# Kernel optimization log

Measured on AMD Instinct MI355X. Metric: run time of the kernel, lower is better.

## Reference

```python
import jax, jax.numpy as jnp
import numpy as np

B, N, T, F = 16, 512, 24, 64


def setup_inputs() -> dict:
    key = jax.random.key(0)
    k1, k2, k3, k4 = jax.random.split(key, 4)
    ori_flow = jax.random.normal(k1, (B, N, T, F), dtype=jnp.float32)
    uncer = jax.random.normal(k2, (B, N, T, F), dtype=jnp.float32)
    spatial_embedding = jax.random.normal(k3, (N, F), dtype=jnp.float32)
    # nn.Linear(channels, channels, bias=False): y = x @ W.T, W: (out, in)
    W1 = jax.random.normal(k4, (F, F), dtype=jnp.float32) * (1.0 / np.sqrt(F))
    return {"ori_flow": ori_flow, "uncer": uncer,
            "spatial_embedding": spatial_embedding, "W1": W1}


def reference(ori_flow, uncer, spatial_embedding, W1):
    b, n, t, f = ori_flow.shape
    # (B, N, T, f) -> (B*T, N, f)
    x = ori_flow.transpose(0, 2, 1, 3).reshape(-1, n, f)
    u = uncer.transpose(0, 2, 1, 3).reshape(-1, n, f)
    # spatial embedding is identical across batch and time after expand/permute
    emb = jnp.broadcast_to(spatial_embedding, (b * t, n, f))
    h = jnp.concatenate([x, emb], axis=-1)            # (B*T, N, 2f)
    rel = jax.nn.relu(jnp.einsum('bnf,bmf->bnm', h, h))  # (B*T, N, N)
    rel = jax.nn.softmax(rel, axis=-1)                # dropout p=0 -> identity
    # sharing_paras=True: both branches use linear1 (no bias)
    of = jax.nn.relu(jnp.einsum('bnm,bmf->bnf', rel, x) @ W1.T)
    uf = jax.nn.relu(jnp.einsum('bnm,bmf->bnf', rel, u) @ W1.T)
    of = of.reshape(b, t, n, f).transpose(0, 2, 1, 3)  # (B, N, T, f)
    uf = uf.reshape(b, t, n, f).transpose(0, 2, 1, 3)
    return of, uf
```

## Files before the change

### kernel.cpp

```cpp
#include <hip/hip_runtime.h>
#include <hip/hip_bf16.h>

#define BB 16
#define NN 512
#define TT 24
#define FF 64
#define OUT_OFF ((size_t)BB*NN*TT*FF)

#define AIS 136
#define XTS 72
#define XTSZ 4672

typedef __attribute__((ext_vector_type(8))) short v8s;
typedef __attribute__((ext_vector_type(16))) float v16f;

union U16x8 { uint4 v; unsigned short s[8]; };

__device__ inline v16f mfma32(v8s a, v8s b, v16f c) {
    return __builtin_amdgcn_mfma_f32_32x32x16_bf16(a, b, c, 0, 0, 0);
}

__device__ inline unsigned int fbits(float x) {
    union { float f; unsigned int u; } c; c.f = x; return c.u;
}
__device__ inline float ibits(unsigned int u) {
    union { float f; unsigned int u; } c; c.u = u; return c.f;
}
__device__ inline unsigned short f2bf_r(float x) {
    return (unsigned short)((fbits(x) + 0x8000u) >> 16);
}
__device__ inline float bf2f(unsigned short u) {
    return ibits(((unsigned int)u) << 16);
}
__device__ inline void split8(const float* f, U16x8& H, U16x8& L) {
    #pragma unroll
    for (int k = 0; k < 8; ++k) {
        unsigned int u  = fbits(f[k]);
        unsigned int hr = (u + 0x8000u) & 0xffff0000u;
        H.s[k] = (unsigned short)(hr >> 16);
        float lo = f[k] - ibits(hr);
        L.s[k] = (unsigned short)((fbits(lo) + 0x8000u) >> 16);
    }
}
__device__ inline void cvt8h(const float* f, U16x8& H) {
    #pragma unroll
    for (int k = 0; k < 8; ++k) H.s[k] = f2bf_r(f[k]);
}

__device__ inline unsigned int pkbf(float a, float b) {
    unsigned int r;
    asm("v_cvt_pk_bf16_f32 %0, %1, %2" : "=v"(r) : "v"(a), "v"(b));
    return r;
}

__device__ inline v8s pfrag(const float* cr, int c) {
    unsigned int a0 = pkbf(cr[8*c+0], cr[8*c+1]);
    unsigned int a1 = pkbf(cr[8*c+2], cr[8*c+3]);
    unsigned int b0 = pkbf(cr[8*c+4], cr[8*c+5]);
    unsigned int b1 = pkbf(cr[8*c+6], cr[8*c+7]);
    asm("v_permlane32_swap_b32 %0, %1" : "+v"(a0), "+v"(b0));
    asm("v_permlane32_swap_b32 %0, %1" : "+v"(a1), "+v"(b1));
    union { v8s v; unsigned int u[4]; } P;
    P.u[0] = a0; P.u[1] = a1; P.u[2] = b0; P.u[3] = b1;
    return P.v;
}

__global__ __launch_bounds__(256, 2)
void spag_kernel(const float* __restrict__ ori, const float* __restrict__ unc,
                 const float* __restrict__ emb, const float* __restrict__ W1,
                 float* __restrict__ out)
{
    __shared__ __align__(16) unsigned short SH[2*64*AIS + 2*XTSZ];
    unsigned short* AjH = SH;
    unsigned short* AjL = SH + 64*AIS;
    unsigned short* XT  = SH + 2*64*AIS;
    unsigned short* UT  = XT + XTSZ;

    const int tid  = threadIdx.x;
    const int bt   = blockIdx.x >> 2;
    const int it   = blockIdx.x & 3;
    const int b    = bt / TT, t = bt % TT;
    const int i0   = it * 128;

    const int lane = tid & 63;
    const int w    = tid >> 6;
    const int m    = lane & 31;
    const int hi   = lane >> 5;

    v8s bH[8], bL[8];
    #pragma unroll
    for (int p = 0; p < 2; ++p) {
        {
            const int sr = tid >> 2, fc = (tid & 3) * 16;
            const float* xb = ori + ((size_t)((b*NN + i0 + p*64 + sr)*TT + t))*FF + fc;
            const float* eb = emb + (size_t)(i0 + p*64 + sr)*FF + fc;
            float tf[8]; U16x8 H, L;
            #pragma unroll
            for (int h = 0; h < 2; ++h) {
                *(float4*)&tf[0] = ((const float4*)xb)[2*h];
                *(float4*)&tf[4] = ((const float4*)xb)[2*h+1];
                split8(tf, H, L);
                *(uint4*)&AjH[sr*AIS + fc + h*8] = H.v;
                *(uint4*)&AjL[sr*AIS + fc + h*8] = L.v;
                *(float4*)&tf[0] = ((const float4*)eb)[2*h];
                *(float4*)&tf[4] = ((const float4*)eb)[2*h+1];
                split8(tf, H, L);
                *(uint4*)&AjH[sr*AIS + 64 + fc + h*8] = H.v;
                *(uint4*)&AjL[sr*AIS + 64 + fc + h*8] = L.v;
            }
        }
        __syncthreads();
        if ((w >> 1) == p) {
            const int lr = (w & 1)*32 + m;
            #pragma unroll
            for (int kk = 0; kk < 8; ++kk) {
                bH[kk] = *(const v8s*)&AjH[lr*AIS + kk*16 + hi*8];
                bL[kk] = *(const v8s*)&AjL[lr*AIS + kk*16 + hi*8];
            }
        }
        __syncthreads();
    }

    v16f accX0 = (v16f)(0.0f), accX1 = (v16f)(0.0f);
    v16f accU0 = (v16f)(0.0f), accU1 = (v16f)(0.0f);
    float rs    = 0.0f;
    float m_run = 0.0f;

    for (int jt = 0; jt < 8; ++jt) {
        const int j0 = jt * 64;
        __syncthreads();

        {
            const int pj = tid >> 3;
            const int f0 = (tid & 7) * 8;
            const int j  = 2 * pj;
            const size_t r0 = ((size_t)((b*NN + j0 + j)*TT + t))*FF + f0;
            const size_t r1 = r0 + (size_t)TT*FF;
            float t0[8], t1[8]; U16x8 H0, L0, H1, L1;

            *(float4*)&t0[0] = *(const float4*)(ori + r0);
            *(float4*)&t0[4] = *(const float4*)(ori + r0 + 4);
            *(float4*)&t1[0] = *(const float4*)(ori + r1);
            *(float4*)&t1[4] = *(const float4*)(ori + r1 + 4);
            split8(t0, H0, L0); split8(t1, H1, L1);
            *(uint4*)&AjH[ j   *AIS + f0] = H0.v;
            *(uint4*)&AjH[(j+1)*AIS + f0] = H1.v;
            *(uint4*)&AjL[ j   *AIS + f0] = L0.v;
            *(uint4*)&AjL[(j+1)*AIS + f0] = L1.v;
            #pragma unroll
            for (int k = 0; k < 8; ++k) {
                int f = f0 + k;
                int off = f*XTS + (f>>4)*16 + j;
                *(unsigned int*)&XT[off] =
                    (unsigned int)H0.s[k] | ((unsigned int)H1.s[k] << 16);
            }
            const float* e0 = emb + (size_t)(j0 + j)*FF + f0;
            *(float4*)&t0[0] = *(const float4*)(e0);
            *(float4*)&t0[4] = *(const float4*)(e0 + 4);
            *(float4*)&t1[0] = *(const float4*)(e0 + FF);
            *(float4*)&t1[4] = *(const float4*)(e0 + FF + 4);
            split8(t0, H0, L0); split8(t1, H1, L1);
            *(uint4*)&AjH[ j   *AIS + 64 + f0] = H0.v;
            *(uint4*)&AjH[(j+1)*AIS + 64 + f0] = H1.v;
            *(uint4*)&AjL[ j   *AIS + 64 + f0] = L0.v;
            *(uint4*)&AjL[(j+1)*AIS + 64 + f0] = L1.v;
            *(float4*)&t0[0] = *(const float4*)(unc + r0);
            *(float4*)&t0[4] = *(const float4*)(unc + r0 + 4);
            *(float4*)&t1[0] = *(const float4*)(unc + r1);
            *(float4*)&t1[4] = *(const float4*)(unc + r1 + 4);
            #pragma unroll
            for (int k = 0; k < 8; ++k) {
                int f = f0 + k;
                int off = f*XTS + (f>>4)*16 + j;
                *(unsigned int*)&UT[off] =
                    (unsigned int)f2bf_r(t0[k]) | ((unsigned int)f2bf_r(t1[k]) << 16);
            }
        }
        __syncthreads();

        v16f C0 = (v16f)(0.0f), C1 = (v16f)(0.0f);
        #pragma unroll
        for (int kk = 0; kk < 8; ++kk) {
            const int fo = kk*16 + hi*8;
            v8s aH0 = *(const v8s*)&AjH[ m     *AIS + fo];
            v8s aL0 = *(const v8s*)&AjL[ m     *AIS + fo];
            v8s aH1 = *(const v8s*)&AjH[(32+m)*AIS + fo];
            v8s aL1 = *(const v8s*)&AjL[(32+m)*AIS + fo];
            C0 = mfma32(aH0, bH[kk], C0);
            C1 = mfma32(aH1, bH[kk], C1);
            C0 = mfma32(aH0, bL[kk], C0);
            C1 = mfma32(aH1, bL[kk], C1);
            C0 = mfma32(aL0, bH[kk], C0);
            C1 = mfma32(aL1, bH[kk], C1);
        }

        float mt = 0.0f;
        #pragma unroll
        for (int r = 0; r < 16; ++r) {
            float s0 = fmaxf(C0[r], 0.0f); C0[r] = s0;
            float s1 = fmaxf(C1[r], 0.0f); C1[r] = s1;
            mt = fmaxf(mt, fmaxf(s0, s1));
        }
        mt = fmaxf(mt, __shfl_xor(mt, 32));
        if (!__all(mt <= m_run + 8.0f)) {
            float m_new = fmaxf(m_run, mt);
            float al = __expf(m_run - m_new);
            rs *= al; m_run = m_new;
            #pragma unroll
            for (int r = 0; r < 16; ++r) {
                float a = __shfl(al, (r & 3) + 8*(r >> 2) + 4*hi);
                accX0[r] *= a; accX1[r] *= a;
                accU0[r] *= a; accU1[r] *= a;
            }
        }

        v8s P[4];
        {
            float cr[16];
            #pragma unroll
            for (int r = 0; r < 16; ++r) {
                float e = __expf(C0[r] - m_run);
                cr[r] = ibits((fbits(e) + 0x8000u) & 0xffff0000u);
                rs += cr[r];
            }
            P[0] = pfrag(cr, 0);
            P[1] = pfrag(cr, 1);
            #pragma unroll
            for (int r = 0; r < 16; ++r) {
                float e = __expf(C1[r] - m_run);
                cr[r] = ibits((fbits(e) + 0x8000u) & 0xffff0000u);
                rs += cr[r];
            }
            P[2] = pfrag(cr, 0);
            P[3] = pfrag(cr, 1);
        }

        #pragma unroll
        for (int kk = 0; kk < 4; ++kk) {
            const int fo = kk*16 + hi*8;
            v8s bx0 = *(const v8s*)&XT[ m     *XTS + (( m    )>>4)*16 + fo];
            v8s bu0 = *(const v8s*)&UT[ m     *XTS + (( m    )>>4)*16 + fo];
            v8s bx1 = *(const v8s*)&XT[(32+m)*XTS + (((32+m))>>4)*16 + fo];
            v8s bu1 = *(const v8s*)&UT[(32+m)*XTS + (((32+m))>>4)*16 + fo];
            accX0 = mfma32(P[kk], bx0, accX0);
            accX1 = mfma32(P[kk], bx1, accX1);
            accU0 = mfma32(P[kk], bu0, accU0);
            accU1 = mfma32(P[kk], bu1, accU1);
        }
    }

    __syncthreads();
    rs += __shfl_xor(rs, 32);
    float inv = 1.0f / rs;

    unsigned short* Ox = SH;
    unsigned short* Ou = SH + 128*XTS;
    unsigned short* Wt = SH + 256*XTS;

    #pragma unroll
    for (int r = 0; r < 16; ++r) {
        int il = (r & 3) + 8*(r >> 2) + 4*hi;
        float iv = __shfl(inv, il);
        int row = w*32 + il;
        Ox[row*XTS + m]      = f2bf_r(accX0[r] * iv);
        Ox[row*XTS + 32 + m] = f2bf_r(accX1[r] * iv);
        Ou[row*XTS + m]      = f2bf_r(accU0[r] * iv);
        Ou[row*XTS + 32 + m] = f2bf_r(accU1[r] * iv);
    }
    {
        const int sr = tid >> 2, fc = (tid & 3) * 16;
        const float* wb = W1 + sr*FF + fc;
        float tf[8]; U16x8 H;
        #pragma unroll
        for (int h = 0; h < 2; ++h) {
            *(float4*)&tf[0] = ((const float4*)wb)[2*h];
            *(float4*)&tf[4] = ((const float4*)wb)[2*h+1];
            cvt8h(tf, H);
            *(uint4*)&Wt[sr*XTS + fc + h*8] = H.v;
        }
    }
    __syncthreads();

    v8s ao[4], aq[4];
    #pragma unroll
    for (int kk = 0; kk < 4; ++kk) {
        const int fo = kk*16 + hi*8;
        ao[kk] = *(const v8s*)&Ox[(w*32 + m)*XTS + fo];
        aq[kk] = *(const v8s*)&Ou[(w*32 + m)*XTS + fo];
    }
    #pragma unroll
    for (int ot = 0; ot < 2; ++ot) {
        v16f ax = (v16f)(0.0f), au = (v16f)(0.0f);
        #pragma unroll
        for (int kk = 0; kk < 4; ++kk) {
            const int fo = kk*16 + hi*8;
            v8s bw = *(const v8s*)&Wt[(ot*32 + m)*XTS + fo];
            ax = mfma32(ao[kk], bw, ax);
            au = mfma32(aq[kk], bw, au);
        }
        #pragma unroll
        for (int r = 0; r < 16; ++r) {
            int il = (r & 3) + 8*(r >> 2) + 4*hi;
            int i = i0 + w*32 + il;
            int o = ot*32 + m;
            size_t idx = ((size_t)((b*NN + i)*TT + t))*FF + o;
            out[idx]           = fmaxf(ax[r], 0.0f);
            out[OUT_OFF + idx] = fmaxf(au[r], 0.0f);
        }
    }
}

extern "C" void kernel_launch(void* const* d_in, const int* in_sizes, int n_in,
                              void* d_out, int out_size, void* d_ws, size_t ws_size,
                              hipStream_t stream) {
    const float* ori = (const float*)d_in[0];
    const float* unc = (const float*)d_in[1];
    const float* emb = (const float*)d_in[2];
    const float* W1  = (const float*)d_in[3];
    float* out = (float*)d_out;

    spag_kernel<<<dim3(BB*TT*4), dim3(256), 0, stream>>>(ori, unc, emb, W1, out);
}
```

Before: 268.2 us.

## Halve j-tile to 32 rows to cut LDS and raise occupancy

Shrinks the key tile from 64 to 32 rows per iteration, halving the shared-memory buffers. The launch bound rises from 2 to 5 blocks per CU and per-thread accumulator state drops. The epilogue is restructured so the W1 projection fits the smaller LDS by processing row halves in two passes. In exchange the main loop runs twice as many iterations with twice as many barriers, and each tile load is smaller.

```diff
diff --git a/kernel.cpp b/kernel.cpp
--- a/kernel.cpp
+++ b/kernel.cpp
@@ -8,13 +8,17 @@
 #define OUT_OFF ((size_t)BB*NN*TT*FF)
 
 #define AIS 136
-#define XTS 72
-#define XTSZ 4672
+#define XTS 56
+#define AJSZ (32*AIS)
+#define XTSZ (64*XTS+16)
+#define OS   72
+#define EOS  (64*OS+16)
 
 typedef __attribute__((ext_vector_type(8))) short v8s;
 typedef __attribute__((ext_vector_type(16))) float v16f;
 
 union U16x8 { uint4 v; unsigned short s[8]; };
+union U16x4 { uint2 v; unsigned short s[4]; };
 
 __device__ inline v16f mfma32(v8s a, v8s b, v16f c) {
     return __builtin_amdgcn_mfma_f32_32x32x16_bf16(a, b, c, 0, 0, 0);
@@ -29,22 +33,15 @@
 __device__ inline unsigned short f2bf_r(float x) {
     return (unsigned short)((fbits(x) + 0x8000u) >> 16);
 }
-__device__ inline float bf2f(unsigned short u) {
-    return ibits(((unsigned int)u) << 16);
-}
-__device__ inline void split8(const float* f, U16x8& H, U16x8& L) {
+__device__ inline void split4(const float* f, U16x4& H, U16x4& L) {
     #pragma unroll
-    for (int k = 0; k < 8; ++k) {
+    for (int k = 0; k < 4; ++k) {
         unsigned int u  = fbits(f[k]);
         unsigned int hr = (u + 0x8000u) & 0xffff0000u;
         H.s[k] = (unsigned short)(hr >> 16);
         float lo = f[k] - ibits(hr);
         L.s[k] = (unsigned short)((fbits(lo) + 0x8000u) >> 16);
     }
-}
-__device__ inline void cvt8h(const float* f, U16x8& H) {
-    #pragma unroll
-    for (int k = 0; k < 8; ++k) H.s[k] = f2bf_r(f[k]);
 }
 
 __device__ inline unsigned int pkbf(float a, float b) {
@@ -65,15 +62,15 @@
     return P.v;
 }
 
-__global__ __launch_bounds__(256, 2)
+__global__ __launch_bounds__(256, 5)
 void spag_kernel(const float* __restrict__ ori, const float* __restrict__ unc,
                  const float* __restrict__ emb, const float* __restrict__ W1,
                  float* __restrict__ out)
 {
-    __shared__ __align__(16) unsigned short SH[2*64*AIS + 2*XTSZ];
+    __shared__ __align__(16) unsigned short SH[2*AJSZ + 2*XTSZ];
     unsigned short* AjH = SH;
-    unsigned short* AjL = SH + 64*AIS;
-    unsigned short* XT  = SH + 2*64*AIS;
+    unsigned short* AjL = SH + AJSZ;
+    unsigned short* XT  = SH + 2*AJSZ;
     unsigned short* UT  = XT + XTSZ;
 
     const int tid  = threadIdx.x;
@@ -87,35 +84,38 @@
     const int m    = lane & 31;
     const int hi   = lane >> 5;
 
+    const int pr = tid >> 4;
+    const int f0 = (tid & 15) * 4;
+    const int jl = 2 * pr;
+
     v8s bH[8], bL[8];
     #pragma unroll
-    for (int p = 0; p < 2; ++p) {
+    for (int p = 0; p < 4; ++p) {
         {
-            const int sr = tid >> 2, fc = (tid & 3) * 16;
-            const float* xb = ori + ((size_t)((b*NN + i0 + p*64 + sr)*TT + t))*FF + fc;
-            const float* eb = emb + (size_t)(i0 + p*64 + sr)*FF + fc;
-            float tf[8]; U16x8 H, L;
-            #pragma unroll
-            for (int h = 0; h < 2; ++h) {
-                *(float4*)&tf[0] = ((const float4*)xb)[2*h];
-                *(float4*)&tf[4] = ((const float4*)xb)[2*h+1];
-                split8(tf, H, L);
-                *(uint4*)&AjH[sr*AIS + fc + h*8] = H.v;
-                *(uint4*)&AjL[sr*AIS + fc + h*8] = L.v;
-                *(float4*)&tf[0] = ((const float4*)eb)[2*h];
-                *(float4*)&tf[4] = ((const float4*)eb)[2*h+1];
-                split8(tf, H, L);
-                *(uint4*)&AjH[sr*AIS + 64 + fc + h*8] = H.v;
-                *(uint4*)&AjL[sr*AIS + 64 + fc + h*8] = L.v;
-            }
-        }
-        __syncthreads();
-        if ((w >> 1) == p) {
-            const int lr = (w & 1)*32 + m;
+            const int gi = i0 + p*32 + jl;
+            const float* xb = ori + ((size_t)((b*NN + gi)*TT + t))*FF + f0;
+            const float* eb = emb + (size_t)gi*FF + f0;
+            float a0[4], a1[4], e0[4], e1[4];
+            *(float4*)a0 = *(const float4*)xb;
+            *(float4*)a1 = *(const float4*)(xb + (size_t)TT*FF);
+            *(float4*)e0 = *(const float4*)eb;
+            *(float4*)e1 = *(const float4*)(eb + FF);
+            U16x4 H, L;
+            split4(a0, H, L);
+            *(uint2*)&AjH[ jl   *AIS + f0] = H.v;  *(uint2*)&AjL[ jl   *AIS + f0] = L.v;
+            split4(a1, H, L);
+            *(uint2*)&AjH[(jl+1)*AIS + f0] = H.v;  *(uint2*)&AjL[(jl+1)*AIS + f0] = L.v;
+            split4(e0, H, L);
+            *(uint2*)&AjH[ jl   *AIS + 64 + f0] = H.v;  *(uint2*)&AjL[ jl   *AIS + 64 + f0] = L.v;
+            split4(e1, H, L);
+            *(uint2*)&AjH[(jl+1)*AIS + 64 + f0] = H.v;  *(uint2*)&AjL[(jl+1)*AIS + 64 + f0] = L.v;
+        }
+        __syncthreads();
+        if (w == p) {
             #pragma unroll
             for (int kk = 0; kk < 8; ++kk) {
-                bH[kk] = *(const v8s*)&AjH[lr*AIS + kk*16 + hi*8];
-                bL[kk] = *(const v8s*)&AjL[lr*AIS + kk*16 + hi*8];
+                bH[kk] = *(const v8s*)&AjH[m*AIS + kk*16 + hi*8];
+                bL[kk] = *(const v8s*)&AjL[m*AIS + kk*16 + hi*8];
             }
         }
         __syncthreads();
@@ -126,80 +126,63 @@
     float rs    = 0.0f;
     float m_run = 0.0f;
 
-    for (int jt = 0; jt < 8; ++jt) {
-        const int j0 = jt * 64;
+    for (int jt = 0; jt < 16; ++jt) {
+        const int j0 = jt * 32;
         __syncthreads();
 
         {
-            const int pj = tid >> 3;
-            const int f0 = (tid & 7) * 8;
-            const int j  = 2 * pj;
-            const size_t r0 = ((size_t)((b*NN + j0 + j)*TT + t))*FF + f0;
+            const int gj = j0 + jl;
+            const size_t r0 = ((size_t)((b*NN + gj)*TT + t))*FF + f0;
             const size_t r1 = r0 + (size_t)TT*FF;
-            float t0[8], t1[8]; U16x8 H0, L0, H1, L1;
-
-            *(float4*)&t0[0] = *(const float4*)(ori + r0);
-            *(float4*)&t0[4] = *(const float4*)(ori + r0 + 4);
-            *(float4*)&t1[0] = *(const float4*)(ori + r1);
-            *(float4*)&t1[4] = *(const float4*)(ori + r1 + 4);
-            split8(t0, H0, L0); split8(t1, H1, L1);
-            *(uint4*)&AjH[ j   *AIS + f0] = H0.v;
-            *(uint4*)&AjH[(j+1)*AIS + f0] = H1.v;
-            *(uint4*)&AjL[ j   *AIS + f0] = L0.v;
-            *(uint4*)&AjL[(j+1)*AIS + f0] = L1.v;
-            #pragma unroll
-            for (int k = 0; k < 8; ++k) {
+            const float* ep = emb + (size_t)gj*FF + f0;
+            float a0[4], a1[4], e0[4], e1[4], u0[4], u1[4];
+            *(float4*)a0 = *(const float4*)(ori + r0);
+            *(float4*)a1 = *(const float4*)(ori + r1);
+            *(float4*)e0 = *(const float4*)(ep);
+            *(float4*)e1 = *(const float4*)(ep + FF);
+            *(float4*)u0 = *(const float4*)(unc + r0);
+            *(float4*)u1 = *(const float4*)(unc + r1);
+
+            U16x4 H0, L0, H1, L1;
+            split4(a0, H0, L0); split4(a1, H1, L1);
+            *(uint2*)&AjH[ jl   *AIS + f0] = H0.v;  *(uint2*)&AjL[ jl   *AIS + f0] = L0.v;
+            *(uint2*)&AjH[(jl+1)*AIS + f0] = H1.v;  *(uint2*)&AjL[(jl+1)*AIS + f0] = L1.v;
+            #pragma unroll
+            for (int k = 0; k < 4; ++k) {
                 int f = f0 + k;
-                int off = f*XTS + (f>>4)*16 + j;
+                int off = f*XTS + ((f>>4)&1)*16 + jl;
                 *(unsigned int*)&XT[off] =
                     (unsigned int)H0.s[k] | ((unsigned int)H1.s[k] << 16);
             }
-            const float* e0 = emb + (size_t)(j0 + j)*FF + f0;
-            *(float4*)&t0[0] = *(const float4*)(e0);
-            *(float4*)&t0[4] = *(const float4*)(e0 + 4);
-            *(float4*)&t1[0] = *(const float4*)(e0 + FF);
-            *(float4*)&t1[4] = *(const float4*)(e0 + FF + 4);
-            split8(t0, H0, L0); split8(t1, H1, L1);
-            *(uint4*)&AjH[ j   *AIS + 64 + f0] = H0.v;
-            *(uint4*)&AjH[(j+1)*AIS + 64 + f0] = H1.v;
-            *(uint4*)&AjL[ j   *AIS + 64 + f0] = L0.v;
-            *(uint4*)&AjL[(j+1)*AIS + 64 + f0] = L1.v;
-            *(float4*)&t0[0] = *(const float4*)(unc + r0);
-            *(float4*)&t0[4] = *(const float4*)(unc + r0 + 4);
-            *(float4*)&t1[0] = *(const float4*)(unc + r1);
-            *(float4*)&t1[4] = *(const float4*)(unc + r1 + 4);
-            #pragma unroll
-            for (int k = 0; k < 8; ++k) {
+            split4(e0, H0, L0); split4(e1, H1, L1);
+            *(uint2*)&AjH[ jl   *AIS + 64 + f0] = H0.v;  *(uint2*)&AjL[ jl   *AIS + 64 + f0] = L0.v;
+            *(uint2*)&AjH[(jl+1)*AIS + 64 + f0] = H1.v;  *(uint2*)&AjL[(jl+1)*AIS + 64 + f0] = L1.v;
+            #pragma unroll
+            for (int k = 0; k < 4; ++k) {
                 int f = f0 + k;
-                int off = f*XTS + (f>>4)*16 + j;
+                int off = f*XTS + ((f>>4)&1)*16 + jl;
                 *(unsigned int*)&UT[off] =
-                    (unsigned int)f2bf_r(t0[k]) | ((unsigned int)f2bf_r(t1[k]) << 16);
-            }
-        }
-        __syncthreads();
-
-        v16f C0 = (v16f)(0.0f), C1 = (v16f)(0.0f);
+                    (unsigned int)f2bf_r(u0[k]) | ((unsigned int)f2bf_r(u1[k]) << 16);
+            }
+        }
+        __syncthreads();
+
+        v16f C = (v16f)(0.0f);
         #pragma unroll
         for (int kk = 0; kk < 8; ++kk) {
             const int fo = kk*16 + hi*8;
-            v8s aH0 = *(const v8s*)&AjH[ m     *AIS + fo];
-            v8s aL0 = *(const v8s*)&AjL[ m     *AIS + fo];
-            v8s aH1 = *(const v8s*)&AjH[(32+m)*AIS + fo];
-            v8s aL1 = *(const v8s*)&AjL[(32+m)*AIS + fo];
-            C0 = mfma32(aH0, bH[kk], C0);
-            C1 = mfma32(aH1, bH[kk], C1);
-            C0 = mfma32(aH0, bL[kk], C0);
-            C1 = mfma32(aH1, bL[kk], C1);
-            C0 = mfma32(aL0, bH[kk], C0);
-            C1 = mfma32(aL1, bH[kk], C1);
+            v8s aH = *(const v8s*)&AjH[m*AIS + fo];
+            v8s aL = *(const v8s*)&AjL[m*AIS + fo];
+            C = mfma32(aH, bH[kk], C);
+            C = mfma32(aH, bL[kk], C);
+            C = mfma32(aL, bH[kk], C);
         }
 
         float mt = 0.0f;
         #pragma unroll
         for (int r = 0; r < 16; ++r) {
-            float s0 = fmaxf(C0[r], 0.0f); C0[r] = s0;
-            float s1 = fmaxf(C1[r], 0.0f); C1[r] = s1;
-            mt = fmaxf(mt, fmaxf(s0, s1));
+            float s = fmaxf(C[r], 0.0f); C[r] = s;
+            mt = fmaxf(mt, s);
         }
         mt = fmaxf(mt, __shfl_xor(mt, 32));
         if (!__all(mt <= m_run + 8.0f)) {
@@ -214,34 +197,26 @@
             }
         }
 
-        v8s P[4];
+        v8s P[2];
         {
             float cr[16];
             #pragma unroll
             for (int r = 0; r < 16; ++r) {
-                float e = __expf(C0[r] - m_run);
+                float e = __expf(C[r] - m_run);
                 cr[r] = ibits((fbits(e) + 0x8000u) & 0xffff0000u);
                 rs += cr[r];
             }
             P[0] = pfrag(cr, 0);
             P[1] = pfrag(cr, 1);
-            #pragma unroll
-            for (int r = 0; r < 16; ++r) {
-                float e = __expf(C1[r] - m_run);
-                cr[r] = ibits((fbits(e) + 0x8000u) & 0xffff0000u);
-                rs += cr[r];
-            }
-            P[2] = pfrag(cr, 0);
-            P[3] = pfrag(cr, 1);
-        }
-
-        #pragma unroll
-        for (int kk = 0; kk < 4; ++kk) {
+        }
+
+        #pragma unroll
+        for (int kk = 0; kk < 2; ++kk) {
             const int fo = kk*16 + hi*8;
-            v8s bx0 = *(const v8s*)&XT[ m     *XTS + (( m    )>>4)*16 + fo];
-            v8s bu0 = *(const v8s*)&UT[ m     *XTS + (( m    )>>4)*16 + fo];
-            v8s bx1 = *(const v8s*)&XT[(32+m)*XTS + (((32+m))>>4)*16 + fo];
-            v8s bu1 = *(const v8s*)&UT[(32+m)*XTS + (((32+m))>>4)*16 + fo];
+            v8s bx0 = *(const v8s*)&XT[ m    *XTS + (( m    >>4)&1)*16 + fo];
+            v8s bu0 = *(const v8s*)&UT[ m    *XTS + (( m    >>4)&1)*16 + fo];
+            v8s bx1 = *(const v8s*)&XT[(32+m)*XTS + (((32+m)>>4)&1)*16 + fo];
+            v8s bu1 = *(const v8s*)&UT[(32+m)*XTS + (((32+m)>>4)&1)*16 + fo];
             accX0 = mfma32(P[kk], bx0, accX0);
             accX1 = mfma32(P[kk], bx1, accX1);
             accU0 = mfma32(P[kk], bu0, accU0);
@@ -254,55 +229,56 @@
     float inv = 1.0f / rs;
 
     unsigned short* Ox = SH;
-    unsigned short* Ou = SH + 128*XTS;
-    unsigned short* Wt = SH + 256*XTS;
-
-    #pragma unroll
-    for (int r = 0; r < 16; ++r) {
-        int il = (r & 3) + 8*(r >> 2) + 4*hi;
-        float iv = __shfl(inv, il);
-        int row = w*32 + il;
-        Ox[row*XTS + m]      = f2bf_r(accX0[r] * iv);
-        Ox[row*XTS + 32 + m] = f2bf_r(accX1[r] * iv);
-        Ou[row*XTS + m]      = f2bf_r(accU0[r] * iv);
-        Ou[row*XTS + 32 + m] = f2bf_r(accU1[r] * iv);
-    }
+    unsigned short* Ou = SH + EOS;
+    unsigned short* Wt = SH + 2*EOS;
+
     {
         const int sr = tid >> 2, fc = (tid & 3) * 16;
         const float* wb = W1 + sr*FF + fc;
-        float tf[8]; U16x8 H;
-        #pragma unroll
-        for (int h = 0; h < 2; ++h) {
-            *(float4*)&tf[0] = ((const float4*)wb)[2*h];
-            *(float4*)&tf[4] = ((const float4*)wb)[2*h+1];
-            cvt8h(tf, H);
-            *(uint4*)&Wt[sr*XTS + fc + h*8] = H.v;
-        }
-    }
-    __syncthreads();
-
-    v8s ao[4], aq[4];
+        #pragma unroll
+        for (int h = 0; h < 4; ++h) {
+            float tf[4];
+            *(float4*)tf = ((const float4*)wb)[h];
+            U16x4 H;
+            #pragma unroll
+            for (int k = 0; k < 4; ++k) H.s[k] = f2bf_r(tf[k]);
+            *(uint2*)&Wt[sr*OS + fc + h*4] = H.v;
+        }
+    }
+
     #pragma unroll
-    for (int kk = 0; kk < 4; ++kk) {
-        const int fo = kk*16 + hi*8;
-        ao[kk] = *(const v8s*)&Ox[(w*32 + m)*XTS + fo];
-        aq[kk] = *(const v8s*)&Ou[(w*32 + m)*XTS + fo];
-    }
-    #pragma unroll
-    for (int ot = 0; ot < 2; ++ot) {
+    for (int p = 0; p < 2; ++p) {
+        if (p) __syncthreads();
+        if ((w >> 1) == p) {
+            #pragma unroll
+            for (int r = 0; r < 16; ++r) {
+                int il = (r & 3) + 8*(r >> 2) + 4*hi;
+                float iv = __shfl(inv, il);
+                int row = (w & 1)*32 + il;
+                Ox[row*OS + m]      = f2bf_r(accX0[r] * iv);
+                Ox[row*OS + 32 + m] = f2bf_r(accX1[r] * iv);
+                Ou[row*OS + m]      = f2bf_r(accU0[r] * iv);
+                Ou[row*OS + 32 + m] = f2bf_r(accU1[r] * iv);
+            }
+        }
+        __syncthreads();
+
+        const int ri = w & 1, ro = w >> 1;
         v16f ax = (v16f)(0.0f), au = (v16f)(0.0f);
         #pragma unroll
         for (int kk = 0; kk < 4; ++kk) {
             const int fo = kk*16 + hi*8;
-            v8s bw = *(const v8s*)&Wt[(ot*32 + m)*XTS + fo];
-            ax = mfma32(ao[kk], bw, ax);
-            au = mfma32(aq[kk], bw, au);
+            v8s ao = *(const v8s*)&Ox[(ri*32 + m)*OS + fo];
+            v8s aq = *(const v8s*)&Ou[(ri*32 + m)*OS + fo];
+            v8s bw = *(const v8s*)&Wt[(ro*32 + m)*OS + fo];
+            ax = mfma32(ao, bw, ax);
+            au = mfma32(aq, bw, au);
         }
         #pragma unroll
         for (int r = 0; r < 16; ++r) {
             int il = (r & 3) + 8*(r >> 2) + 4*hi;
-            int i = i0 + w*32 + il;
-            int o = ot*32 + m;
+            int i = i0 + p*64 + ri*32 + il;
+            int o = ro*32 + m;
             size_t idx = ((size_t)((b*NN + i)*TT + t))*FF + o;
             out[idx]           = fmaxf(ax[r], 0.0f);
             out[OUT_OFF + idx] = fmaxf(au[r], 0.0f);
```

After: 986.9 us. 3.68x slower.

## Prefetch next j-tile into registers and remap blocks per XCD

Applied to the files above, without the earlier changes.

Loads of the next 64-row tile of ori and uncer are issued into registers right after the LDS barrier, so their global latency overlaps the MFMA work of the current tile. Block indices are also remapped so that consecutive blocks on the same XCD share a (b,t) slice, which is meant to improve L2 reuse of the repeatedly read key/value rows. The cost is 32 extra live VGPRs under a 2-waves-per-EU launch bound, which risks spills or lower occupancy. The XCD remap assumes 8 XCDs and a grid of 1536 blocks.

```diff
diff --git a/kernel.cpp b/kernel.cpp
--- a/kernel.cpp
+++ b/kernel.cpp
@@ -28,9 +28,6 @@
 }
 __device__ inline unsigned short f2bf_r(float x) {
     return (unsigned short)((fbits(x) + 0x8000u) >> 16);
-}
-__device__ inline float bf2f(unsigned short u) {
-    return ibits(((unsigned int)u) << 16);
 }
 __device__ inline void split8(const float* f, U16x8& H, U16x8& L) {
     #pragma unroll
@@ -77,8 +74,10 @@
     unsigned short* UT  = XT + XTSZ;
 
     const int tid  = threadIdx.x;
-    const int bt   = blockIdx.x >> 2;
-    const int it   = blockIdx.x & 3;
+    const int xcd  = blockIdx.x & 7;
+    const int slot = blockIdx.x >> 3;
+    const int bt   = xcd * 48 + (slot >> 2);
+    const int it   = slot & 3;
     const int b    = bt / TT, t = bt % TT;
     const int i0   = it * 128;
 
@@ -86,6 +85,24 @@
     const int w    = tid >> 6;
     const int m    = lane & 31;
     const int hi   = lane >> 5;
+
+    const int pj  = tid >> 3;
+    const int f0  = (tid & 7) * 8;
+    const int jme = 2 * pj;
+
+    float pa0[8], pa1[8], pu0[8], pu1[8];
+    {
+        const size_t r0 = ((size_t)((b*NN + jme)*TT + t))*FF + f0;
+        const size_t r1 = r0 + (size_t)TT*FF;
+        *(float4*)&pa0[0] = *(const float4*)(ori + r0);
+        *(float4*)&pa0[4] = *(const float4*)(ori + r0 + 4);
+        *(float4*)&pa1[0] = *(const float4*)(ori + r1);
+        *(float4*)&pa1[4] = *(const float4*)(ori + r1 + 4);
+        *(float4*)&pu0[0] = *(const float4*)(unc + r0);
+        *(float4*)&pu0[4] = *(const float4*)(unc + r0 + 4);
+        *(float4*)&pu1[0] = *(const float4*)(unc + r1);
+        *(float4*)&pu1[4] = *(const float4*)(unc + r1 + 4);
+    }
 
     v8s bH[8], bL[8];
     #pragma unroll
@@ -131,18 +148,9 @@
         __syncthreads();
 
         {
-            const int pj = tid >> 3;
-            const int f0 = (tid & 7) * 8;
-            const int j  = 2 * pj;
-            const size_t r0 = ((size_t)((b*NN + j0 + j)*TT + t))*FF + f0;
-            const size_t r1 = r0 + (size_t)TT*FF;
-            float t0[8], t1[8]; U16x8 H0, L0, H1, L1;
-
-            *(float4*)&t0[0] = *(const float4*)(ori + r0);
-            *(float4*)&t0[4] = *(const float4*)(ori + r0 + 4);
-            *(float4*)&t1[0] = *(const float4*)(ori + r1);
-            *(float4*)&t1[4] = *(const float4*)(ori + r1 + 4);
-            split8(t0, H0, L0); split8(t1, H1, L1);
+            const int j = jme;
+            U16x8 H0, L0, H1, L1;
+            split8(pa0, H0, L0); split8(pa1, H1, L1);
             *(uint4*)&AjH[ j   *AIS + f0] = H0.v;
             *(uint4*)&AjH[(j+1)*AIS + f0] = H1.v;
             *(uint4*)&AjL[ j   *AIS + f0] = L0.v;
@@ -154,7 +162,15 @@
                 *(unsigned int*)&XT[off] =
                     (unsigned int)H0.s[k] | ((unsigned int)H1.s[k] << 16);
             }
+            #pragma unroll
+            for (int k = 0; k < 8; ++k) {
+                int f = f0 + k;
+                int off = f*XTS + (f>>4)*16 + j;
+                *(unsigned int*)&UT[off] =
+                    (unsigned int)f2bf_r(pu0[k]) | ((unsigned int)f2bf_r(pu1[k]) << 16);
+            }
             const float* e0 = emb + (size_t)(j0 + j)*FF + f0;
+            float t0[8], t1[8];
             *(float4*)&t0[0] = *(const float4*)(e0);
             *(float4*)&t0[4] = *(const float4*)(e0 + 4);
             *(float4*)&t1[0] = *(const float4*)(e0 + FF);
@@ -164,19 +180,21 @@
             *(uint4*)&AjH[(j+1)*AIS + 64 + f0] = H1.v;
             *(uint4*)&AjL[ j   *AIS + 64 + f0] = L0.v;
             *(uint4*)&AjL[(j+1)*AIS + 64 + f0] = L1.v;
-            *(float4*)&t0[0] = *(const float4*)(unc + r0);
-            *(float4*)&t0[4] = *(const float4*)(unc + r0 + 4);
-            *(float4*)&t1[0] = *(const float4*)(unc + r1);
-            *(float4*)&t1[4] = *(const float4*)(unc + r1 + 4);
-            #pragma unroll
-            for (int k = 0; k < 8; ++k) {
-                int f = f0 + k;
-                int off = f*XTS + (f>>4)*16 + j;
-                *(unsigned int*)&UT[off] =
-                    (unsigned int)f2bf_r(t0[k]) | ((unsigned int)f2bf_r(t1[k]) << 16);
-            }
         }
         __syncthreads();
+
+        if (jt < 7) {
+            const size_t r0 = ((size_t)((b*NN + j0 + 64 + jme)*TT + t))*FF + f0;
+            const size_t r1 = r0 + (size_t)TT*FF;
+            *(float4*)&pa0[0] = *(const float4*)(ori + r0);
+            *(float4*)&pa0[4] = *(const float4*)(ori + r0 + 4);
+            *(float4*)&pa1[0] = *(const float4*)(ori + r1);
+            *(float4*)&pa1[4] = *(const float4*)(ori + r1 + 4);
+            *(float4*)&pu0[0] = *(const float4*)(unc + r0);
+            *(float4*)&pu0[4] = *(const float4*)(unc + r0 + 4);
+            *(float4*)&pu1[0] = *(const float4*)(unc + r1);
+            *(float4*)&pu1[4] = *(const float4*)(unc + r1 + 4);
+        }
 
         v16f C0 = (v16f)(0.0f), C1 = (v16f)(0.0f);
         #pragma unroll
```

After: 265.1 us. About the same (-1.2%).
